# Kernel optimization log

Measured on AMD Instinct MI355X. Metric: run time of the kernel, lower is better.

Reference implementation:

```python
import jax, jax.numpy as jnp
import numpy as np

D_MODEL = 1024
N_HEAD = 16
D_HEAD = D_MODEL // N_HEAD


def setup_inputs() -> dict:
    key = jax.random.key(0)
    k1, k2, k3 = jax.random.split(key, 3)
    x = jax.random.normal(k1, (4, 1024, D_MODEL), dtype=jnp.float32)
    # torch Linear(d_model, 3*d_model, bias=False): weight [3*d_model, d_model], y = x @ W.T
    w_qkv = jax.random.normal(k2, (3 * D_MODEL, D_MODEL), dtype=jnp.float32) * (1.0 / np.sqrt(D_MODEL))
    w_out = jax.random.normal(k3, (D_MODEL, D_MODEL), dtype=jnp.float32) * (1.0 / np.sqrt(D_MODEL))
    return {"x": x, "w_qkv": w_qkv, "w_out": w_out}


def reference(x, w_qkv, w_out):
    B, T, C = x.shape
    qkv = x @ w_qkv.T                                   # [B,T,3C]
    qkv = qkv.reshape(B, T, 3, N_HEAD, D_HEAD)
    q = jnp.transpose(qkv[:, :, 0], (0, 2, 1, 3))       # [B,H,T,Dh]
    k = jnp.transpose(qkv[:, :, 1], (0, 2, 1, 3))
    v = jnp.transpose(qkv[:, :, 2], (0, 2, 1, 3))
    att = jnp.einsum('bhqd,bhkd->bhqk', q, k) / jnp.sqrt(jnp.float32(D_HEAD))
    causal = jnp.tril(jnp.ones((T, T), dtype=bool))
    att = jnp.where(causal[None, None], att, -jnp.inf)
    att = jax.nn.softmax(att, axis=-1)
    y = jnp.einsum('bhqk,bhkd->bhqd', att, v)           # [B,H,T,Dh]
    y = jnp.transpose(y, (0, 2, 1, 3)).reshape(B, T, C)
    return y @ w_out.T
```

## Files before the change

### kernel.cpp

```cpp
#include <hip/hip_runtime.h>
#include <hip/hip_bf16.h>
#include <stdint.h>

#define DM 1024
#define NH 16
#define DH 64
#define BB 4
#define TT 1024
#define MR (BB*TT)

typedef __attribute__((ext_vector_type(8))) short bf16x8;
typedef __attribute__((ext_vector_type(4))) float f32x4;

typedef unsigned int __attribute__((address_space(1))) uint_g;
typedef unsigned int __attribute__((address_space(3))) uint_l;

static __device__ __forceinline__ void gload_lds16(const void* g, void* l) {
  __builtin_amdgcn_global_load_lds((const uint_g*)g, (uint_l*)l, 16, 0, 0);
}

static __device__ __forceinline__ unsigned short f2bf(float f) {
  union { float f; unsigned int u; } v; v.f = f;
  unsigned int r = v.u + 0x7fffu + ((v.u >> 16) & 1u);
  return (unsigned short)(r >> 16);
}

__global__ __launch_bounds__(256) void k_cvt3(const float* __restrict__ x,
    const float* __restrict__ w1, const float* __restrict__ w2,
    unsigned short* __restrict__ xb, unsigned short* __restrict__ wqb,
    unsigned short* __restrict__ wob) {
  const int n1 = (MR * DM) / 4, n2 = (3 * DM * DM) / 4, n3 = (DM * DM) / 4;
  const int total = n1 + n2 + n3;
  for (int u = blockIdx.x * 256 + threadIdx.x; u < total; u += gridDim.x * 256) {
    const float* src; unsigned short* dst; int i;
    if (u < n1)           { src = x;  dst = xb;  i = u; }
    else if (u < n1 + n2) { src = w1; dst = wqb; i = u - n1; }
    else                  { src = w2; dst = wob; i = u - n1 - n2; }
    float4 v = reinterpret_cast<const float4*>(src)[i];
    ushort4 o;
    o.x = f2bf(v.x); o.y = f2bf(v.y); o.z = f2bf(v.z); o.w = f2bf(v.w);
    reinterpret_cast<ushort4*>(dst)[i] = o;
  }
}

template<int EPI>
__global__ __launch_bounds__(256) void k_gemm(
    const unsigned short* __restrict__ A, const unsigned short* __restrict__ Bw,
    float* __restrict__ Of, unsigned short* __restrict__ qb,
    unsigned short* __restrict__ kb, unsigned short* __restrict__ vtb,
    int N, int K, int tiles_n) {
  __shared__ unsigned short SH[2][2][128 * 32];
  int tid = threadIdx.x;
  int w = tid >> 6, l = tid & 63;
  int l15 = l & 15, k8 = l >> 4;
  int nwg = gridDim.x;
  int cpx = nwg >> 3;
  int wg = blockIdx.x;
  int swz = (wg & 7) * cpx + (wg >> 3);
  int tm = swz / tiles_n, tn = swz % tiles_n;
  int m0 = tm << 7, n0 = tn << 7;

  f32x4 acc[4][4];
  #pragma unroll
  for (int i = 0; i < 4; ++i)
    #pragma unroll
    for (int j = 0; j < 4; ++j) acc[i][j] = (f32x4){0.f, 0.f, 0.f, 0.f};

  int srow = (w << 4) + (l >> 2);
  int sch = l & 3;
  int mrb = ((w >> 1) << 6) + l15;
  int nrb = ((w & 1) << 6) + l15;

  auto stage = [&](int buf, int kk) {
    #pragma unroll
    for (int p = 0; p < 2; ++p) {
      int row = srow + (p << 6);
      int c = sch ^ ((row >> 1) & 3);
      int seg = w + (p << 2);
      gload_lds16(A + (size_t)(m0 + row) * K + kk + (c << 3), &SH[buf][0][seg << 9]);
      gload_lds16(Bw + (size_t)(n0 + row) * K + kk + (c << 3), &SH[buf][1][seg << 9]);
    }
  };

  stage(0, 0);
  __syncthreads();
  int cur = 0;
  for (int kk = 0; kk < K; kk += 32) {
    if (kk + 32 < K) stage(cur ^ 1, kk + 32);
    bf16x8 a[4], b[4];
    #pragma unroll
    for (int mf = 0; mf < 4; ++mf) {
      int row = mrb + (mf << 4);
      a[mf] = *(const bf16x8*)&SH[cur][0][(row << 5) + ((k8 ^ ((row >> 1) & 3)) << 3)];
    }
    #pragma unroll
    for (int nf = 0; nf < 4; ++nf) {
      int row = nrb + (nf << 4);
      b[nf] = *(const bf16x8*)&SH[cur][1][(row << 5) + ((k8 ^ ((row >> 1) & 3)) << 3)];
    }
    #pragma unroll
    for (int mf = 0; mf < 4; ++mf)
      #pragma unroll
      for (int nf = 0; nf < 4; ++nf)
        acc[mf][nf] = __builtin_amdgcn_mfma_f32_16x16x32_bf16(a[mf], b[nf], acc[mf][nf], 0, 0, 0);
    __syncthreads();
    cur ^= 1;
  }

  if (EPI == 1) {
    #pragma unroll
    for (int mf = 0; mf < 4; ++mf)
      #pragma unroll
      for (int nf = 0; nf < 4; ++nf) {
        int n = n0 + ((w & 1) << 6) + (nf << 4) + l15;
        int m_base = m0 + ((w >> 1) << 6) + (mf << 4) + (k8 << 2);
        #pragma unroll
        for (int r = 0; r < 4; ++r)
          Of[(size_t)(m_base + r) * N + n] = acc[mf][nf][r];
      }
    return;
  }

  int s = n0 >> 10;
  if (s < 2) {
    #pragma unroll
    for (int mf = 0; mf < 4; ++mf) {
      #pragma unroll
      for (int nf = 0; nf < 4; ++nf) {
        int n = n0 + ((w & 1) << 6) + (nf << 4) + l15;
        int rem = n & 1023;
        int h = rem >> 6, d = rem & 63;
        int m_base = m0 + ((w >> 1) << 6) + (mf << 4) + (k8 << 2);
        #pragma unroll
        for (int r = 0; r < 4; ++r) {
          int m = m_base + r;
          int bb = m >> 10, t = m & 1023;
          float v = acc[mf][nf][r];
          if (s == 0)
            qb[((size_t)(bb * NH + h) * TT + t) * DH + d] = f2bf(v * 0.18033688f);
          else
            kb[((size_t)(bb * NH + h) * TT + t) * DH + d] = f2bf(v);
        }
      }
    }
  } else {
    unsigned short* T = &SH[0][0][0];
    int bb = m0 >> 10, t0 = m0 & 1023;
    int myhalf = w & 1;
    #pragma unroll
    for (int half = 0; half < 2; ++half) {
      __syncthreads();
      if (myhalf == half) {
        #pragma unroll
        for (int nf = 0; nf < 4; ++nf) {
          int nloc = (nf << 4) + l15;
          #pragma unroll
          for (int mf = 0; mf < 4; ++mf) {
            int mloc = ((w >> 1) << 6) + (mf << 4) + (k8 << 2);
            #pragma unroll
            for (int r = 0; r < 4; ++r)
              T[nloc * 134 + mloc + r] = f2bf(acc[mf][nf][r]);
          }
        }
      }
      __syncthreads();
      {
        int d = tid >> 2, mseg = tid & 3;
        int n = n0 + (half << 6) + d;
        int h = (n & 1023) >> 6;
        size_t base = ((size_t)(bb * NH + h) * DH + d) * TT + t0 + (mseg << 5);
        #pragma unroll
        for (int i = 0; i < 4; ++i) {
          ushort4 v4 = *(const ushort4*)&T[d * 134 + (mseg << 5) + (i << 3)];
          ushort4 v4b = *(const ushort4*)&T[d * 134 + (mseg << 5) + (i << 3) + 4];
          *(ushort4*)&vtb[base + (i << 3)] = v4;
          *(ushort4*)&vtb[base + (i << 3) + 4] = v4b;
        }
      }
    }
  }
}

__global__ __launch_bounds__(256) void k_gemm1(
    const unsigned short* __restrict__ A, const unsigned short* __restrict__ Bw,
    float* __restrict__ Of, int N, int K) {
  __shared__ unsigned short At[2][64 * 32];
  __shared__ unsigned short Bt[2][128 * 32];
  int tid = threadIdx.x;
  int w = tid >> 6, l = tid & 63;
  int l15 = l & 15, k8 = l >> 4;
  int wg = blockIdx.x;
  int swz = (wg & 7) * 64 + (wg >> 3);
  int tm = swz >> 3, tn = swz & 7;
  int m0 = tm << 6, n0 = tn << 7;
  int wm = w >> 1, wn = w & 1;

  f32x4 acc[2][4];
  #pragma unroll
  for (int i = 0; i < 2; ++i)
    #pragma unroll
    for (int j = 0; j < 4; ++j) acc[i][j] = (f32x4){0.f, 0.f, 0.f, 0.f};

  int srl = l >> 2;
  int sch = l & 3;

  auto stage = [&](int buf, int kk) {
    {
      int row = (w << 4) + srl;
      int c = sch ^ ((row >> 1) & 3);
      gload_lds16(A + (size_t)(m0 + row) * K + kk + (c << 3), &At[buf][w << 9]);
    }
    #pragma unroll
    for (int p = 0; p < 2; ++p) {
      int seg = (w << 1) + p;
      int row = (seg << 4) + srl;
      int c = sch ^ ((row >> 1) & 3);
      gload_lds16(Bw + (size_t)(n0 + row) * K + kk + (c << 3), &Bt[buf][seg << 9]);
    }
  };

  stage(0, 0);
  __syncthreads();
  int cur = 0;
  for (int kk = 0; kk < K; kk += 32) {
    if (kk + 32 < K) stage(cur ^ 1, kk + 32);
    bf16x8 a[2], b[4];
    #pragma unroll
    for (int mf = 0; mf < 2; ++mf) {
      int row = (wm << 5) + (mf << 4) + l15;
      a[mf] = *(const bf16x8*)&At[cur][(row << 5) + ((k8 ^ ((row >> 1) & 3)) << 3)];
    }
    #pragma unroll
    for (int nf = 0; nf < 4; ++nf) {
      int row = (wn << 6) + (nf << 4) + l15;
      b[nf] = *(const bf16x8*)&Bt[cur][(row << 5) + ((k8 ^ ((row >> 1) & 3)) << 3)];
    }
    #pragma unroll
    for (int mf = 0; mf < 2; ++mf)
      #pragma unroll
      for (int nf = 0; nf < 4; ++nf)
        acc[mf][nf] = __builtin_amdgcn_mfma_f32_16x16x32_bf16(a[mf], b[nf], acc[mf][nf], 0, 0, 0);
    __syncthreads();
    cur ^= 1;
  }

  #pragma unroll
  for (int mf = 0; mf < 2; ++mf)
    #pragma unroll
    for (int nf = 0; nf < 4; ++nf) {
      int n = n0 + (wn << 6) + (nf << 4) + l15;
      int m_base = m0 + (wm << 5) + (mf << 4) + (k8 << 2);
      #pragma unroll
      for (int r = 0; r < 4; ++r)
        Of[(size_t)(m_base + r) * N + n] = acc[mf][nf][r];
    }
}

__global__ __launch_bounds__(512) void k_attn(
    const unsigned short* __restrict__ qb, const unsigned short* __restrict__ kb,
    const unsigned short* __restrict__ vtb, unsigned short* __restrict__ yb) {
  __shared__ unsigned short Kt[2][64 * 64];
  __shared__ unsigned short Vt[2][64 * 64];
  __shared__ unsigned short Pl[8][16][72];
  int tid = threadIdx.x, w = tid >> 6, l = tid & 63;
  int l15 = l & 15, k8 = l >> 4;
  int bh = blockIdx.x >> 3;
  int a = blockIdx.x & 7;
  int wlo = w & 3;
  int qb_w = (w < 4) ? ((a << 6) + (wlo << 4))
                     : ((TT - ((a + 1) << 6)) + (wlo << 4));
  const unsigned short* Kb = kb + (size_t)bh * TT * DH;
  const unsigned short* Vb = vtb + (size_t)bh * DH * TT;
  const unsigned short* Qb = qb + (size_t)bh * TT * DH;

  int qrow = qb_w + l15;
  bf16x8 qf[2];
  #pragma unroll
  for (int c = 0; c < 2; ++c)
    qf[c] = *(const bf16x8*)&Qb[(size_t)qrow * DH + (c << 5) + (k8 << 3)];

  f32x4 y[4];
  #pragma unroll
  for (int i = 0; i < 4; ++i) y[i] = (f32x4){0.f, 0.f, 0.f, 0.f};
  float lacc = 0.f;

  const float NEG_BIAS = -23.083120654f;
  f32x4 bias4 = {NEG_BIAS, NEG_BIAS, NEG_BIAS, NEG_BIAS};

  int srow = l >> 3;
  int sch = l & 7;

  auto stage = [&](int buf, int j0) {
    int row = (w << 3) + srow;
    int c = sch ^ (row & 7);
    gload_lds16(Kb + (size_t)(j0 + row) * DH + (c << 3), &Kt[buf][(w << 3) << 6]);
    gload_lds16(Vb + (size_t)row * TT + j0 + (c << 3), &Vt[buf][(w << 3) << 6]);
  };

  const int ns = 16 - a;
  stage(0, 0);
  __syncthreads();
  int cur = 0;

  for (int t = 0; t < ns; ++t) {
    int j0 = t << 6;
    if (t + 1 < ns) stage(cur ^ 1, (t + 1) << 6);

    if (j0 <= qb_w + 15) {
      f32x4 s[4];
      #pragma unroll
      for (int f = 0; f < 4; ++f) s[f] = bias4;
      __builtin_amdgcn_s_setprio(1);
      #pragma unroll
      for (int c = 0; c < 2; ++c) {
        #pragma unroll
        for (int f = 0; f < 4; ++f) {
          int row = (f << 4) + l15;
          bf16x8 ak = *(const bf16x8*)&Kt[cur][(row << 6) + ((((c << 2) + k8) ^ (row & 7)) << 3)];
          s[f] = __builtin_amdgcn_mfma_f32_16x16x32_bf16(ak, qf[c], s[f], 0, 0, 0);
        }
      }
      __builtin_amdgcn_s_setprio(0);

      if (j0 + 64 > qb_w) {
        #pragma unroll
        for (int f = 0; f < 4; ++f)
          #pragma unroll
          for (int r = 0; r < 4; ++r)
            if (j0 + (f << 4) + (k8 << 2) + r > qrow) s[f][r] = -INFINITY;
      }

      #pragma unroll
      for (int f = 0; f < 4; ++f)
        #pragma unroll
        for (int r = 0; r < 4; ++r) {
          float p;
          asm("v_exp_f32 %0, %1" : "=v"(p) : "v"(s[f][r]));
          s[f][r] = p;
          lacc += p;
        }

      #pragma unroll
      for (int f = 0; f < 4; ++f) {
        unsigned int lo, hi;
        asm("v_cvt_pk_bf16_f32 %0, %1, %2" : "=v"(lo) : "v"(s[f][0]), "v"(s[f][1]));
        asm("v_cvt_pk_bf16_f32 %0, %1, %2" : "=v"(hi) : "v"(s[f][2]), "v"(s[f][3]));
        uint2 pk2; pk2.x = lo; pk2.y = hi;
        *(uint2*)&Pl[w][l15][(f << 4) + (k8 << 2)] = pk2;
      }
      asm volatile("s_waitcnt lgkmcnt(0)" ::: "memory");
      __builtin_amdgcn_sched_barrier(0);

      __builtin_amdgcn_s_setprio(1);
      #pragma unroll
      for (int c = 0; c < 2; ++c) {
        bf16x8 bp = *(const bf16x8*)&Pl[w][l15][(c << 5) + (k8 << 3)];
        #pragma unroll
        for (int mf = 0; mf < 4; ++mf) {
          int dr = (mf << 4) + l15;
          bf16x8 av = *(const bf16x8*)&Vt[cur][(dr << 6) + ((((c << 2) + k8) ^ (dr & 7)) << 3)];
          y[mf] = __builtin_amdgcn_mfma_f32_16x16x32_bf16(av, bp, y[mf], 0, 0, 0);
        }
      }
      __builtin_amdgcn_s_setprio(0);
    }

    __syncthreads();
    cur ^= 1;
  }

  lacc += __shfl_xor(lacc, 16, 64);
  lacc += __shfl_xor(lacc, 32, 64);
  float inv = 1.f / lacc;
  int bb = bh >> 4, h = bh & 15;
  #pragma unroll
  for (int mf = 0; mf < 4; ++mf) {
    ushort4 o;
    o.x = f2bf(y[mf][0] * inv);
    o.y = f2bf(y[mf][1] * inv);
    o.z = f2bf(y[mf][2] * inv);
    o.w = f2bf(y[mf][3] * inv);
    *(ushort4*)&yb[((size_t)(bb * TT + qrow) << 10) + (h << 6) + (mf << 4) + (k8 << 2)] = o;
  }
}

extern "C" void kernel_launch(void* const* d_in, const int* in_sizes, int n_in,
                              void* d_out, int out_size, void* d_ws, size_t ws_size,
                              hipStream_t stream) {
  const float* x    = (const float*)d_in[0];
  const float* wqkv = (const float*)d_in[1];
  const float* wout = (const float*)d_in[2];
  char* ws = (char*)d_ws;
  unsigned short* xb  = (unsigned short*)(ws + (size_t)0);
  unsigned short* wqb = (unsigned short*)(ws + ((size_t)8  << 20));
  unsigned short* wob = (unsigned short*)(ws + ((size_t)14 << 20));
  unsigned short* qbv = (unsigned short*)(ws + ((size_t)16 << 20));
  unsigned short* kbv = (unsigned short*)(ws + ((size_t)24 << 20));
  unsigned short* vtb = (unsigned short*)(ws + ((size_t)32 << 20));
  unsigned short* yb  = (unsigned short*)(ws + ((size_t)40 << 20));

  k_cvt3<<<2048, 256, 0, stream>>>(x, wqkv, wout, xb, wqb, wob);
  k_gemm<0><<<768, 256, 0, stream>>>(xb, wqb, nullptr, qbv, kbv, vtb, 3 * DM, DM, 24);
  k_attn<<<512, 512, 0, stream>>>(qbv, kbv, vtb, yb);
  k_gemm1<<<512, 256, 0, stream>>>(yb, wob, (float*)d_out, DM, DM);
}
```

Baseline: 92.37 us.

## Process two query tiles per wave and triple-buffer K/V in attention

Each attention wave now handles 32 query rows as two 16-row groups that share each K and V fragment read from LDS, so LDS traffic per MFMA is halved. The grid drops from 512 to 256 blocks. K/V staging moves from double to triple buffering with explicit vmcnt waits and raw s_barrier, so loads run two tiles ahead. The cost is more registers per wave and fewer blocks (256) on a GPU with 256 CUs, which may leave occupancy and load balance worse.

```diff
diff --git a/kernel.cpp b/kernel.cpp
--- a/kernel.cpp
+++ b/kernel.cpp
@@ -18,6 +18,8 @@
 static __device__ __forceinline__ void gload_lds16(const void* g, void* l) {
   __builtin_amdgcn_global_load_lds((const uint_g*)g, (uint_l*)l, 16, 0, 0);
 }
+
+static __device__ __forceinline__ void fence() { asm volatile("" ::: "memory"); }
 
 static __device__ __forceinline__ unsigned short f2bf(float f) {
   union { float f; unsigned int u; } v; v.f = f;
@@ -259,30 +261,33 @@
 __global__ __launch_bounds__(512) void k_attn(
     const unsigned short* __restrict__ qb, const unsigned short* __restrict__ kb,
     const unsigned short* __restrict__ vtb, unsigned short* __restrict__ yb) {
-  __shared__ unsigned short Kt[2][64 * 64];
-  __shared__ unsigned short Vt[2][64 * 64];
-  __shared__ unsigned short Pl[8][16][72];
+  __shared__ unsigned short Kt[3][64 * 64];
+  __shared__ unsigned short Vt[3][64 * 64];
+  __shared__ unsigned short Pl[8][2][16][72];
   int tid = threadIdx.x, w = tid >> 6, l = tid & 63;
   int l15 = l & 15, k8 = l >> 4;
-  int bh = blockIdx.x >> 3;
-  int a = blockIdx.x & 7;
+  int bh = blockIdx.x >> 2;
+  int a = blockIdx.x & 3;
   int wlo = w & 3;
-  int qb_w = (w < 4) ? ((a << 6) + (wlo << 4))
-                     : ((TT - ((a + 1) << 6)) + (wlo << 4));
+  int qb_w = (w < 4) ? ((a << 7) + (wlo << 5))
+                     : ((TT - ((a + 1) << 7)) + (wlo << 5));
   const unsigned short* Kb = kb + (size_t)bh * TT * DH;
   const unsigned short* Vb = vtb + (size_t)bh * DH * TT;
   const unsigned short* Qb = qb + (size_t)bh * TT * DH;
 
-  int qrow = qb_w + l15;
-  bf16x8 qf[2];
-  #pragma unroll
-  for (int c = 0; c < 2; ++c)
-    qf[c] = *(const bf16x8*)&Qb[(size_t)qrow * DH + (c << 5) + (k8 << 3)];
-
-  f32x4 y[4];
-  #pragma unroll
-  for (int i = 0; i < 4; ++i) y[i] = (f32x4){0.f, 0.f, 0.f, 0.f};
-  float lacc = 0.f;
+  bf16x8 qf[2][2];
+  #pragma unroll
+  for (int g = 0; g < 2; ++g)
+    #pragma unroll
+    for (int c = 0; c < 2; ++c)
+      qf[g][c] = *(const bf16x8*)&Qb[(size_t)(qb_w + (g << 4) + l15) * DH + (c << 5) + (k8 << 3)];
+
+  f32x4 y[2][4];
+  #pragma unroll
+  for (int g = 0; g < 2; ++g)
+    #pragma unroll
+    for (int i = 0; i < 4; ++i) y[g][i] = (f32x4){0.f, 0.f, 0.f, 0.f};
+  float lacc0 = 0.f, lacc1 = 0.f;
 
   const float NEG_BIAS = -23.083120654f;
   f32x4 bias4 = {NEG_BIAS, NEG_BIAS, NEG_BIAS, NEG_BIAS};
@@ -297,90 +302,113 @@
     gload_lds16(Vb + (size_t)row * TT + j0 + (c << 3), &Vt[buf][(w << 3) << 6]);
   };
 
-  const int ns = 16 - a;
+  const int ns = 16 - (a << 1);
   stage(0, 0);
-  __syncthreads();
-  int cur = 0;
-
+  stage(1, 64);
+  asm volatile("s_waitcnt vmcnt(2)" ::: "memory");
+  fence(); __builtin_amdgcn_s_barrier(); fence();
+
+  int rd = 0;
   for (int t = 0; t < ns; ++t) {
     int j0 = t << 6;
-    if (t + 1 < ns) stage(cur ^ 1, (t + 1) << 6);
-
-    if (j0 <= qb_w + 15) {
-      f32x4 s[4];
-      #pragma unroll
-      for (int f = 0; f < 4; ++f) s[f] = bias4;
+    int st = (rd == 0) ? 2 : rd - 1;
+    if (t + 2 < ns) stage(st, (t + 2) << 6);
+
+    if (j0 <= qb_w + 31) {
+      f32x4 s[2][4];
+      #pragma unroll
+      for (int g = 0; g < 2; ++g)
+        #pragma unroll
+        for (int f = 0; f < 4; ++f) s[g][f] = bias4;
       __builtin_amdgcn_s_setprio(1);
       #pragma unroll
       for (int c = 0; c < 2; ++c) {
         #pragma unroll
         for (int f = 0; f < 4; ++f) {
           int row = (f << 4) + l15;
-          bf16x8 ak = *(const bf16x8*)&Kt[cur][(row << 6) + ((((c << 2) + k8) ^ (row & 7)) << 3)];
-          s[f] = __builtin_amdgcn_mfma_f32_16x16x32_bf16(ak, qf[c], s[f], 0, 0, 0);
+          bf16x8 ak = *(const bf16x8*)&Kt[rd][(row << 6) + ((((c << 2) + k8) ^ (row & 7)) << 3)];
+          s[0][f] = __builtin_amdgcn_mfma_f32_16x16x32_bf16(ak, qf[0][c], s[0][f], 0, 0, 0);
+          s[1][f] = __builtin_amdgcn_mfma_f32_16x16x32_bf16(ak, qf[1][c], s[1][f], 0, 0, 0);
         }
       }
       __builtin_amdgcn_s_setprio(0);
 
       if (j0 + 64 > qb_w) {
         #pragma unroll
-        for (int f = 0; f < 4; ++f)
+        for (int g = 0; g < 2; ++g) {
+          int qrow_g = qb_w + (g << 4) + l15;
           #pragma unroll
-          for (int r = 0; r < 4; ++r)
-            if (j0 + (f << 4) + (k8 << 2) + r > qrow) s[f][r] = -INFINITY;
+          for (int f = 0; f < 4; ++f)
+            #pragma unroll
+            for (int r = 0; r < 4; ++r)
+              if (j0 + (f << 4) + (k8 << 2) + r > qrow_g) s[g][f][r] = -INFINITY;
+        }
       }
 
       #pragma unroll
       for (int f = 0; f < 4; ++f)
         #pragma unroll
         for (int r = 0; r < 4; ++r) {
-          float p;
-          asm("v_exp_f32 %0, %1" : "=v"(p) : "v"(s[f][r]));
-          s[f][r] = p;
-          lacc += p;
-        }
-
-      #pragma unroll
-      for (int f = 0; f < 4; ++f) {
-        unsigned int lo, hi;
-        asm("v_cvt_pk_bf16_f32 %0, %1, %2" : "=v"(lo) : "v"(s[f][0]), "v"(s[f][1]));
-        asm("v_cvt_pk_bf16_f32 %0, %1, %2" : "=v"(hi) : "v"(s[f][2]), "v"(s[f][3]));
-        uint2 pk2; pk2.x = lo; pk2.y = hi;
-        *(uint2*)&Pl[w][l15][(f << 4) + (k8 << 2)] = pk2;
-      }
+          float p0, p1;
+          asm("v_exp_f32 %0, %1" : "=v"(p0) : "v"(s[0][f][r]));
+          asm("v_exp_f32 %0, %1" : "=v"(p1) : "v"(s[1][f][r]));
+          s[0][f][r] = p0; lacc0 += p0;
+          s[1][f][r] = p1; lacc1 += p1;
+        }
+
+      #pragma unroll
+      for (int g = 0; g < 2; ++g)
+        #pragma unroll
+        for (int f = 0; f < 4; ++f) {
+          unsigned int lo, hi;
+          asm("v_cvt_pk_bf16_f32 %0, %1, %2" : "=v"(lo) : "v"(s[g][f][0]), "v"(s[g][f][1]));
+          asm("v_cvt_pk_bf16_f32 %0, %1, %2" : "=v"(hi) : "v"(s[g][f][2]), "v"(s[g][f][3]));
+          uint2 pk2; pk2.x = lo; pk2.y = hi;
+          *(uint2*)&Pl[w][g][l15][(f << 4) + (k8 << 2)] = pk2;
+        }
       asm volatile("s_waitcnt lgkmcnt(0)" ::: "memory");
       __builtin_amdgcn_sched_barrier(0);
 
       __builtin_amdgcn_s_setprio(1);
       #pragma unroll
       for (int c = 0; c < 2; ++c) {
-        bf16x8 bp = *(const bf16x8*)&Pl[w][l15][(c << 5) + (k8 << 3)];
+        bf16x8 bp0 = *(const bf16x8*)&Pl[w][0][l15][(c << 5) + (k8 << 3)];
+        bf16x8 bp1 = *(const bf16x8*)&Pl[w][1][l15][(c << 5) + (k8 << 3)];
         #pragma unroll
         for (int mf = 0; mf < 4; ++mf) {
           int dr = (mf << 4) + l15;
-          bf16x8 av = *(const bf16x8*)&Vt[cur][(dr << 6) + ((((c << 2) + k8) ^ (dr & 7)) << 3)];
-          y[mf] = __builtin_amdgcn_mfma_f32_16x16x32_bf16(av, bp, y[mf], 0, 0, 0);
+          bf16x8 av = *(const bf16x8*)&Vt[rd][(dr << 6) + ((((c << 2) + k8) ^ (dr & 7)) << 3)];
+          y[0][mf] = __builtin_amdgcn_mfma_f32_16x16x32_bf16(av, bp0, y[0][mf], 0, 0, 0);
+          y[1][mf] = __builtin_amdgcn_mfma_f32_16x16x32_bf16(av, bp1, y[1][mf], 0, 0, 0);
         }
       }
       __builtin_amdgcn_s_setprio(0);
     }
 
-    __syncthreads();
-    cur ^= 1;
-  }
-
-  lacc += __shfl_xor(lacc, 16, 64);
-  lacc += __shfl_xor(lacc, 32, 64);
-  float inv = 1.f / lacc;
+    if (t + 2 < ns)      { asm volatile("s_waitcnt vmcnt(2)" ::: "memory"); }
+    else if (t + 1 < ns) { asm volatile("s_waitcnt vmcnt(0)" ::: "memory"); }
+    fence(); __builtin_amdgcn_s_barrier(); fence();
+    rd = (rd == 2) ? 0 : rd + 1;
+  }
+
+  lacc0 += __shfl_xor(lacc0, 16, 64);
+  lacc0 += __shfl_xor(lacc0, 32, 64);
+  lacc1 += __shfl_xor(lacc1, 16, 64);
+  lacc1 += __shfl_xor(lacc1, 32, 64);
   int bb = bh >> 4, h = bh & 15;
   #pragma unroll
-  for (int mf = 0; mf < 4; ++mf) {
-    ushort4 o;
-    o.x = f2bf(y[mf][0] * inv);
-    o.y = f2bf(y[mf][1] * inv);
-    o.z = f2bf(y[mf][2] * inv);
-    o.w = f2bf(y[mf][3] * inv);
-    *(ushort4*)&yb[((size_t)(bb * TT + qrow) << 10) + (h << 6) + (mf << 4) + (k8 << 2)] = o;
+  for (int g = 0; g < 2; ++g) {
+    float inv = 1.f / (g ? lacc1 : lacc0);
+    int qrow_g = qb_w + (g << 4) + l15;
+    #pragma unroll
+    for (int mf = 0; mf < 4; ++mf) {
+      ushort4 o;
+      o.x = f2bf(y[g][mf][0] * inv);
+      o.y = f2bf(y[g][mf][1] * inv);
+      o.z = f2bf(y[g][mf][2] * inv);
+      o.w = f2bf(y[g][mf][3] * inv);
+      *(ushort4*)&yb[((size_t)(bb * TT + qrow_g) << 10) + (h << 6) + (mf << 4) + (k8 << 2)] = o;
+    }
   }
 }
 
@@ -401,6 +429,6 @@
 
   k_cvt3<<<2048, 256, 0, stream>>>(x, wqkv, wout, xb, wqb, wob);
   k_gemm<0><<<768, 256, 0, stream>>>(xb, wqb, nullptr, qbv, kbv, vtb, 3 * DM, DM, 24);
-  k_attn<<<512, 512, 0, stream>>>(qbv, kbv, vtb, yb);
+  k_attn<<<256, 512, 0, stream>>>(qbv, kbv, vtb, yb);
   k_gemm1<<<512, 256, 0, stream>>>(yb, wob, (float*)d_out, DM, DM);
 }
```

Result: no change. 94.13 us (+1.9%).
